# Kernel tuning notes

Hardware: AMD Instinct MI355X
Metric: run time of the kernel (lower is better)

Reference implementation:

```python
import jax, jax.numpy as jnp
import numpy as np

N, DEG, IN_DIM, HID, OUT = 50000, 32, 256, 256, 128

def setup_inputs() -> dict:
    key = jax.random.key(0)
    k1, k2, k3, k4, k5, k6 = jax.random.split(key, 6)
    node_features = jax.random.normal(k1, (N, IN_DIM), dtype=jnp.float32)
    neighbor_idx = jax.random.randint(k2, (N, DEG), 0, N)
    scale1 = 1.0 / np.sqrt(2 * IN_DIM)
    scale2 = 1.0 / np.sqrt(HID)
    W1 = jax.random.normal(k3, (HID, 2 * IN_DIM), dtype=jnp.float32) * scale1
    b1 = jax.random.normal(k4, (HID,), dtype=jnp.float32) * scale1
    W2 = jax.random.normal(k5, (OUT, HID), dtype=jnp.float32) * scale2
    b2 = jax.random.normal(k6, (OUT,), dtype=jnp.float32) * scale2
    return {"node_features": node_features, "neighbor_idx": neighbor_idx,
            "W1": W1, "b1": b1, "W2": W2, "b2": b2}

def reference(node_features, neighbor_idx, W1, b1, W2, b2):
    # Layer 0 (mean aggregator, with neighbors):
    # gather [N, DEG, IN_DIM] neighbor features, mean over DEG
    nbr_mean = jnp.mean(node_features[neighbor_idx], axis=1)  # [N, IN_DIM]
    combined = jnp.concatenate([node_features, nbr_mean], axis=-1)  # [N, 2*IN_DIM]
    h = jax.nn.relu(combined @ W1.T + b1)  # [N, HID]
    # Layer 1: empty neighbor list -> linear_without_neighbors + relu
    out = jax.nn.relu(h @ W2.T + b2)  # [N, OUT]
    return out
```

## Files before the change

### kernel.cpp

```cpp
#include <hip/hip_runtime.h>
#include <stdint.h>

#define N_NODES 50000
#define DEG     32
#define IN_DIM  256
#define K1      512
#define HID     256
#define OUT_DIM 128

#define NCHUNK  4
#define CDIM    64
#define SLICE8  ((size_t)N_NODES * CDIM)
#define GT      16

#define MT2    64
#define NT2B   ((N_NODES + MT2 - 1) / MT2)
#define KC2    32
#define NKA    16
#define NKB    8
#define HSTR2  264

typedef __bf16 bf16x8 __attribute__((ext_vector_type(8)));
typedef float  f32x4  __attribute__((ext_vector_type(4)));
typedef float  f32x2  __attribute__((ext_vector_type(2)));

__device__ __forceinline__ unsigned short f2bf(float f) {
    union { float f; unsigned u; } v; v.f = f;
    unsigned r = v.u + 0x7fffu + ((v.u >> 16) & 1u);
    return (unsigned short)(r >> 16);
}
__device__ __forceinline__ int clampN(int v) {
    return v < 0 ? 0 : (v >= N_NODES ? N_NODES - 1 : v);
}
__device__ __forceinline__ void async_copy16(const void* g, void* l) {
    __builtin_amdgcn_global_load_lds(
        (const __attribute__((address_space(1))) void*)g,
        (__attribute__((address_space(3))) void*)l, 16, 0, 0);
}

#define FEAT_BLKS ((N_NODES + 7) / 8)
__global__ __launch_bounds__(256)
void prep_all(const float* __restrict__ feat,
              const float* __restrict__ W1, const float* __restrict__ W2,
              const int*   __restrict__ nbr,
              unsigned short* __restrict__ featb,
              unsigned char*  __restrict__ featF8,
              unsigned short* __restrict__ W1b, unsigned short* __restrict__ W2b,
              unsigned short* __restrict__ nbr16)
{
    const int t = threadIdx.x;
    if (blockIdx.x < FEAT_BLKS) {
        const int node = blockIdx.x * 8 + (t >> 5);
        const int seg  = t & 31;
        if (node < N_NODES) {
            const float4* src = (const float4*)(feat + (size_t)node * IN_DIM + seg * 8);
            float4 f0 = src[0], f1 = src[1];
            ushort4 o0, o1;
            o0.x = f2bf(f0.x); o0.y = f2bf(f0.y); o0.z = f2bf(f0.z); o0.w = f2bf(f0.w);
            o1.x = f2bf(f1.x); o1.y = f2bf(f1.y); o1.z = f2bf(f1.z); o1.w = f2bf(f1.w);
            unsigned short* db = featb + (size_t)node * IN_DIM + seg * 8;
            *(ushort4*)db       = o0;
            *(ushort4*)(db + 4) = o1;
            int u0 = 0, u1 = 0;
            u0 = __builtin_amdgcn_cvt_pk_fp8_f32(f0.x, f0.y, u0, false);
            u0 = __builtin_amdgcn_cvt_pk_fp8_f32(f0.z, f0.w, u0, true);
            u1 = __builtin_amdgcn_cvt_pk_fp8_f32(f1.x, f1.y, u1, false);
            u1 = __builtin_amdgcn_cvt_pk_fp8_f32(f1.z, f1.w, u1, true);
            const int c   = seg >> 3;
            const int off = (seg & 7) * 8;
            unsigned char* d8 = featF8 + (size_t)c * SLICE8 + (size_t)node * CDIM + off;
            ((int*)d8)[0] = u0;
            ((int*)d8)[1] = u1;
        }
    } else {
        const int bid = blockIdx.x - FEAT_BLKS;
        const int stride = 256 * 256 * 4;
        const int tid4 = (bid * 256 + t) * 4;
        for (int i = tid4; i < HID * K1; i += stride) {
            float4 f = *(const float4*)(W1 + i);
            ushort4 o; o.x = f2bf(f.x); o.y = f2bf(f.y); o.z = f2bf(f.z); o.w = f2bf(f.w);
            *(ushort4*)(W1b + i) = o;
        }
        for (int i = tid4; i < OUT_DIM * HID; i += stride) {
            float4 f = *(const float4*)(W2 + i);
            ushort4 o; o.x = f2bf(f.x); o.y = f2bf(f.y); o.z = f2bf(f.z); o.w = f2bf(f.w);
            *(ushort4*)(W2b + i) = o;
        }
        for (int i = tid4; i < N_NODES * DEG; i += stride) {
            int4 v = *(const int4*)(nbr + i);
            ushort4 o;
            o.x = (unsigned short)clampN(v.x); o.y = (unsigned short)clampN(v.y);
            o.z = (unsigned short)clampN(v.z); o.w = (unsigned short)clampN(v.w);
            *(ushort4*)(nbr16 + i) = o;
        }
    }
}

__global__ __launch_bounds__(256)
void gather_mean_fp8(const unsigned char*  __restrict__ featF8,
                     const unsigned short* __restrict__ nbr16,
                     unsigned short*       __restrict__ meanb)
{
    __shared__ unsigned short sIdx[GT * DEG];
    const int tid  = threadIdx.x;
    const int c    = blockIdx.y;
    const int base = blockIdx.x * GT;

    if (tid < 128) {
        *(ushort4*)(sIdx + tid * 4) =
            *(const ushort4*)(nbr16 + (size_t)base * DEG + tid * 4);
    }
    __syncthreads();

    const unsigned char* slice = featF8 + (size_t)c * SLICE8;
    const int grp = tid >> 4;
    const int ln  = tid & 15;
    const unsigned short* idxr = sIdx + grp * DEG;

    unsigned vv[DEG];
    #pragma unroll
    for (int j = 0; j < DEG; ++j) {
        int nb = idxr[j];
        vv[j] = *(const unsigned*)(slice + (size_t)nb * CDIM + ln * 4);
    }
    float s0 = 0.f, s1 = 0.f, s2 = 0.f, s3 = 0.f;
    #pragma unroll
    for (int j = 0; j < DEG; ++j) {
        f32x2 lo = __builtin_amdgcn_cvt_pk_f32_fp8(vv[j], false);
        f32x2 hi = __builtin_amdgcn_cvt_pk_f32_fp8(vv[j], true);
        s0 += lo[0]; s1 += lo[1]; s2 += hi[0]; s3 += hi[1];
    }
    const float sc = 1.0f / 32.0f;
    ushort4 o;
    o.x = f2bf(s0 * sc); o.y = f2bf(s1 * sc);
    o.z = f2bf(s2 * sc); o.w = f2bf(s3 * sc);
    const int node = base + grp;
    *(ushort4*)(meanb + (size_t)node * IN_DIM + c * CDIM + ln * 4) = o;
}

__global__ __launch_bounds__(512, 2)
void sage_gemm3(const unsigned short* __restrict__ featb,
                const unsigned short* __restrict__ meanb,
                const unsigned short* __restrict__ W1b,
                const float*          __restrict__ b1,
                const unsigned short* __restrict__ W2b,
                const float*          __restrict__ b2,
                float*                __restrict__ out)
{
    __shared__ __align__(16) unsigned short sA[2][MT2 * KC2];
    __shared__ __align__(16) unsigned short sW[2][256 * KC2];
    __shared__ __align__(16) unsigned short sH[MT2 * HSTR2];

    const int tid  = threadIdx.x;
    const int lane = tid & 63;
    const int wave = tid >> 6;
    const int r    = lane & 15;
    const int q    = lane >> 4;
    const int mh   = wave >> 2;
    const int nq   = wave & 3;
    const int nh   = wave & 3;

    const int tbase = blockIdx.x * MT2;

    const int srow = lane >> 2;
    const int sg   = (lane & 3) ^ (srow & 3);

    auto stageA = [&](int kc, int b) {
        if (wave < 4) {
            const int row  = wave * 16 + srow;
            const int node = clampN(tbase + row);
            const unsigned short* basep = (kc < 8) ? featb : meanb;
            async_copy16(basep + (size_t)node * IN_DIM + (kc & 7) * KC2 + sg * 8,
                         &sA[b][wave * 16 * KC2]);
        }
    };
    auto stageW1 = [&](int kc, int b) {
        #pragma unroll
        for (int j = 0; j < 2; ++j) {
            const int n = wave * 32 + j * 16 + srow;
            async_copy16(W1b + (size_t)n * K1 + kc * KC2 + sg * 8,
                         &sW[b][(wave * 32 + j * 16) * KC2]);
        }
    };
    auto stageW2 = [&](int c, int b) {
        const int n = wave * 16 + srow;
        async_copy16(W2b + (size_t)n * HID + c * KC2 + sg * 8,
                     &sW[b][(wave * 16) * KC2]);
    };

    f32x4 acc1[2][4];
    #pragma unroll
    for (int mt = 0; mt < 2; ++mt)
        #pragma unroll
        for (int nt = 0; nt < 4; ++nt)
            acc1[mt][nt] = (f32x4){0.f, 0.f, 0.f, 0.f};

    stageA(0, 0); stageW1(0, 0);
    __syncthreads();
    int buf = 0;
    for (int kc = 0; kc < NKA; ++kc) {
        if (kc + 1 < NKA) { stageA(kc + 1, buf ^ 1); stageW1(kc + 1, buf ^ 1); }
        else              { stageW2(0, buf ^ 1); }
        {
            const int sl = (q ^ (r & 3)) * 8;
            bf16x8 a[2], w[4];
            #pragma unroll
            for (int mt = 0; mt < 2; ++mt)
                a[mt] = *(const bf16x8*)(&sA[buf][(mh * 32 + mt * 16 + r) * KC2 + sl]);
            #pragma unroll
            for (int nt = 0; nt < 4; ++nt)
                w[nt] = *(const bf16x8*)(&sW[buf][(nq * 64 + nt * 16 + r) * KC2 + sl]);
            #pragma unroll
            for (int mt = 0; mt < 2; ++mt)
                #pragma unroll
                for (int nt = 0; nt < 4; ++nt)
                    acc1[mt][nt] = __builtin_amdgcn_mfma_f32_16x16x32_bf16(
                        a[mt], w[nt], acc1[mt][nt], 0, 0, 0);
        }
        __syncthreads();
        buf ^= 1;
    }

    #pragma unroll
    for (int nt = 0; nt < 4; ++nt) {
        const int n = nq * 64 + nt * 16 + r;
        const float bias = b1[n];
        #pragma unroll
        for (int mt = 0; mt < 2; ++mt)
            #pragma unroll
            for (int g = 0; g < 4; ++g) {
                const int m = mh * 32 + mt * 16 + q * 4 + g;
                float v = acc1[mt][nt][g] + bias;
                sH[m * HSTR2 + n] = f2bf(v > 0.f ? v : 0.f);
            }
    }
    __syncthreads();

    f32x4 acc2[2][2];
    #pragma unroll
    for (int mt = 0; mt < 2; ++mt)
        #pragma unroll
        for (int nt = 0; nt < 2; ++nt)
            acc2[mt][nt] = (f32x4){0.f, 0.f, 0.f, 0.f};

    for (int c = 0; c < NKB; ++c) {
        if (c + 1 < NKB) stageW2(c + 1, buf ^ 1);
        {
            const int sl = (q ^ (r & 3)) * 8;
            bf16x8 h[2], w2[2];
            #pragma unroll
            for (int mt = 0; mt < 2; ++mt)
                h[mt] = *(const bf16x8*)(&sH[(mh * 32 + mt * 16 + r) * HSTR2
                                             + c * KC2 + q * 8]);
            #pragma unroll
            for (int nt = 0; nt < 2; ++nt)
                w2[nt] = *(const bf16x8*)(&sW[buf][(nh * 32 + nt * 16 + r) * KC2 + sl]);
            #pragma unroll
            for (int mt = 0; mt < 2; ++mt)
                #pragma unroll
                for (int nt = 0; nt < 2; ++nt)
                    acc2[mt][nt] = __builtin_amdgcn_mfma_f32_16x16x32_bf16(
                        h[mt], w2[nt], acc2[mt][nt], 0, 0, 0);
        }
        __syncthreads();
        buf ^= 1;
    }

    #pragma unroll
    for (int nt = 0; nt < 2; ++nt) {
        const int o = nh * 32 + nt * 16 + r;
        const float bias = b2[o];
        #pragma unroll
        for (int mt = 0; mt < 2; ++mt)
            #pragma unroll
            for (int g = 0; g < 4; ++g) {
                const int m = mh * 32 + mt * 16 + q * 4 + g;
                const int node = tbase + m;
                if (node < N_NODES) {
                    float v = acc2[mt][nt][g] + bias;
                    out[(size_t)node * OUT_DIM + o] = v > 0.f ? v : 0.f;
                }
            }
    }
}

__global__ __launch_bounds__(256)
void sage_naive(const float* __restrict__ feat, const int* __restrict__ nbr,
                const float* __restrict__ W1, const float* __restrict__ b1,
                const float* __restrict__ W2, const float* __restrict__ b2,
                float* __restrict__ out) {
    __shared__ float comb[K1];
    __shared__ float h[HID];
    const int node = blockIdx.x;
    const int t = threadIdx.x;
    comb[t] = feat[(size_t)node * IN_DIM + t];
    float acc = 0.f;
    for (int d = 0; d < DEG; ++d) {
        int nb = clampN(nbr[node * DEG + d]);
        acc += feat[(size_t)nb * IN_DIM + t];
    }
    comb[IN_DIM + t] = acc * (1.0f / 32.0f);
    __syncthreads();
    float s = b1[t];
    for (int k = 0; k < K1; ++k) s += comb[k] * W1[(size_t)t * K1 + k];
    h[t] = s > 0.f ? s : 0.f;
    __syncthreads();
    if (t < OUT_DIM) {
        float s2 = b2[t];
        for (int k = 0; k < HID; ++k) s2 += h[k] * W2[(size_t)t * HID + k];
        out[(size_t)node * OUT_DIM + t] = s2 > 0.f ? s2 : 0.f;
    }
}

extern "C" void kernel_launch(void* const* d_in, const int* in_sizes, int n_in,
                              void* d_out, int out_size, void* d_ws, size_t ws_size,
                              hipStream_t stream) {
    const float* feat = (const float*)d_in[0];
    const int*   nbr  = (const int*)d_in[1];
    const float* W1   = (const float*)d_in[2];
    const float* b1   = (const float*)d_in[3];
    const float* W2   = (const float*)d_in[4];
    const float* b2   = (const float*)d_in[5];
    float* out = (float*)d_out;

    const size_t feat_elems = (size_t)N_NODES * IN_DIM;
    const size_t w1_elems   = (size_t)HID * K1;
    const size_t w2_elems   = (size_t)OUT_DIM * HID;
    const size_t mean_elems = (size_t)N_NODES * IN_DIM;
    const size_t idx_elems  = (size_t)N_NODES * DEG;
    const size_t u16_elems  = feat_elems + w1_elems + w2_elems + mean_elems + idx_elems;
    const size_t need = u16_elems * sizeof(unsigned short)
                      + (size_t)NCHUNK * SLICE8;

    if (ws_size >= need) {
        unsigned short* featb  = (unsigned short*)d_ws;
        unsigned short* W1b    = featb + feat_elems;
        unsigned short* W2b    = W1b + w1_elems;
        unsigned short* meanb  = W2b + w2_elems;
        unsigned short* nbr16  = meanb + mean_elems;
        unsigned char*  featF8 = (unsigned char*)(nbr16 + idx_elems);

        prep_all<<<FEAT_BLKS + 256, 256, 0, stream>>>(feat, W1, W2, nbr,
                                                      featb, featF8, W1b, W2b, nbr16);
        gather_mean_fp8<<<dim3(N_NODES / GT, NCHUNK), 256, 0, stream>>>(featF8, nbr16, meanb);
        sage_gemm3<<<NT2B, 512, 0, stream>>>(featb, meanb, W1b, b1, W2b, b2, out);
    } else {
        sage_naive<<<N_NODES, 256, 0, stream>>>(feat, nbr, W1, b1, W2, b2, out);
    }
}
```

Before: 178.6 us.

## Widen GEMM K-chunk to 64 and hand-schedule async pipeline with explicit waitcnts

The fused two-layer GEMM kernel now stages K in chunks of 64 instead of 32, using an 8-way XOR swizzle so every wave participates in loading A. The main loop is fully unrolled and uses explicit s_waitcnt vmcnt and s_barrier in place of __syncthreads, so the next chunk's global-to-LDS loads can stay in flight during compute. Bias values are preloaded into registers at kernel start. LDS usage doubles and launch bounds drop to one block per CU, which lowers occupancy. The hand-counted vmcnt values also risk races if the compiler emits other vector memory ops.

```diff
diff --git a/kernel.cpp b/kernel.cpp
--- a/kernel.cpp
+++ b/kernel.cpp
@@ -15,14 +15,17 @@
 
 #define MT2    64
 #define NT2B   ((N_NODES + MT2 - 1) / MT2)
-#define KC2    32
-#define NKA    16
-#define NKB    8
+#define KC3    64
 #define HSTR2  264
 
 typedef __bf16 bf16x8 __attribute__((ext_vector_type(8)));
 typedef float  f32x4  __attribute__((ext_vector_type(4)));
 typedef float  f32x2  __attribute__((ext_vector_type(2)));
+
+#define PIN(x)   asm volatile("" : "+v"(x))
+#define WAITV(N) asm volatile("s_waitcnt vmcnt(" #N ")" ::: "memory")
+#define WAITL()  asm volatile("s_waitcnt lgkmcnt(0)" ::: "memory")
+#define BAR()    asm volatile("s_barrier" ::: "memory")
 
 __device__ __forceinline__ unsigned short f2bf(float f) {
     union { float f; unsigned u; } v; v.f = f;
@@ -138,8 +141,8 @@
     *(ushort4*)(meanb + (size_t)node * IN_DIM + c * CDIM + ln * 4) = o;
 }
 
-__global__ __launch_bounds__(512, 2)
-void sage_gemm3(const unsigned short* __restrict__ featb,
+__global__ __launch_bounds__(512, 1)
+void sage_gemm4(const unsigned short* __restrict__ featb,
                 const unsigned short* __restrict__ meanb,
                 const unsigned short* __restrict__ W1b,
                 const float*          __restrict__ b1,
@@ -147,8 +150,8 @@
                 const float*          __restrict__ b2,
                 float*                __restrict__ out)
 {
-    __shared__ __align__(16) unsigned short sA[2][MT2 * KC2];
-    __shared__ __align__(16) unsigned short sW[2][256 * KC2];
+    __shared__ __align__(16) unsigned short sA[2][MT2 * KC3];
+    __shared__ __align__(16) unsigned short sW[2][256 * KC3];
     __shared__ __align__(16) unsigned short sH[MT2 * HSTR2];
 
     const int tid  = threadIdx.x;
@@ -159,33 +162,39 @@
     const int mh   = wave >> 2;
     const int nq   = wave & 3;
     const int nh   = wave & 3;
+    const int lrow = lane >> 3;
+    const int lsl  = lane & 7;
 
     const int tbase = blockIdx.x * MT2;
 
-    const int srow = lane >> 2;
-    const int sg   = (lane & 3) ^ (srow & 3);
+    float bias1[4], bias2v[2];
+    #pragma unroll
+    for (int nt = 0; nt < 4; ++nt) { bias1[nt] = b1[nq * 64 + nt * 16 + r]; PIN(bias1[nt]); }
+    #pragma unroll
+    for (int nt = 0; nt < 2; ++nt) { bias2v[nt] = b2[nh * 32 + nt * 16 + r]; PIN(bias2v[nt]); }
 
     auto stageA = [&](int kc, int b) {
-        if (wave < 4) {
-            const int row  = wave * 16 + srow;
-            const int node = clampN(tbase + row);
-            const unsigned short* basep = (kc < 8) ? featb : meanb;
-            async_copy16(basep + (size_t)node * IN_DIM + (kc & 7) * KC2 + sg * 8,
-                         &sA[b][wave * 16 * KC2]);
-        }
+        const int p    = wave * 8 + lrow;
+        const int node = clampN(tbase + p);
+        const unsigned short* basep = (kc < 4) ? featb : meanb;
+        async_copy16(basep + (size_t)node * IN_DIM + (kc & 3) * KC3 + ((lsl ^ (p & 7)) << 3),
+                     &sA[b][wave * 8 * KC3]);
     };
     auto stageW1 = [&](int kc, int b) {
         #pragma unroll
+        for (int j = 0; j < 4; ++j) {
+            const int n = wave * 32 + j * 8 + lrow;
+            async_copy16(W1b + (size_t)n * K1 + kc * KC3 + ((lsl ^ (n & 7)) << 3),
+                         &sW[b][(wave * 32 + j * 8) * KC3]);
+        }
+    };
+    auto stageW2 = [&](int c, int b) {
+        #pragma unroll
         for (int j = 0; j < 2; ++j) {
-            const int n = wave * 32 + j * 16 + srow;
-            async_copy16(W1b + (size_t)n * K1 + kc * KC2 + sg * 8,
-                         &sW[b][(wave * 32 + j * 16) * KC2]);
-        }
-    };
-    auto stageW2 = [&](int c, int b) {
-        const int n = wave * 16 + srow;
-        async_copy16(W2b + (size_t)n * HID + c * KC2 + sg * 8,
-                     &sW[b][(wave * 16) * KC2]);
+            const int n = wave * 16 + j * 8 + lrow;
+            async_copy16(W2b + (size_t)n * HID + c * KC3 + ((lsl ^ (n & 7)) << 3),
+                         &sW[b][(wave * 16 + j * 8) * KC3]);
+        }
     };
 
     f32x4 acc1[2][4];
@@ -195,21 +204,17 @@
         for (int nt = 0; nt < 4; ++nt)
             acc1[mt][nt] = (f32x4){0.f, 0.f, 0.f, 0.f};
 
-    stageA(0, 0); stageW1(0, 0);
-    __syncthreads();
-    int buf = 0;
-    for (int kc = 0; kc < NKA; ++kc) {
-        if (kc + 1 < NKA) { stageA(kc + 1, buf ^ 1); stageW1(kc + 1, buf ^ 1); }
-        else              { stageW2(0, buf ^ 1); }
-        {
-            const int sl = (q ^ (r & 3)) * 8;
+    auto computeA = [&](int b) {
+        #pragma unroll
+        for (int kk = 0; kk < 2; ++kk) {
+            const int sl = ((kk * 4 + q) ^ (r & 7)) * 8;
             bf16x8 a[2], w[4];
             #pragma unroll
             for (int mt = 0; mt < 2; ++mt)
-                a[mt] = *(const bf16x8*)(&sA[buf][(mh * 32 + mt * 16 + r) * KC2 + sl]);
+                a[mt] = *(const bf16x8*)(&sA[b][(mh * 32 + mt * 16 + r) * KC3 + sl]);
             #pragma unroll
             for (int nt = 0; nt < 4; ++nt)
-                w[nt] = *(const bf16x8*)(&sW[buf][(nq * 64 + nt * 16 + r) * KC2 + sl]);
+                w[nt] = *(const bf16x8*)(&sW[b][(nq * 64 + nt * 16 + r) * KC3 + sl]);
             #pragma unroll
             for (int mt = 0; mt < 2; ++mt)
                 #pragma unroll
@@ -217,24 +222,7 @@
                     acc1[mt][nt] = __builtin_amdgcn_mfma_f32_16x16x32_bf16(
                         a[mt], w[nt], acc1[mt][nt], 0, 0, 0);
         }
-        __syncthreads();
-        buf ^= 1;
-    }
-
-    #pragma unroll
-    for (int nt = 0; nt < 4; ++nt) {
-        const int n = nq * 64 + nt * 16 + r;
-        const float bias = b1[n];
-        #pragma unroll
-        for (int mt = 0; mt < 2; ++mt)
-            #pragma unroll
-            for (int g = 0; g < 4; ++g) {
-                const int m = mh * 32 + mt * 16 + q * 4 + g;
-                float v = acc1[mt][nt][g] + bias;
-                sH[m * HSTR2 + n] = f2bf(v > 0.f ? v : 0.f);
-            }
-    }
-    __syncthreads();
+    };
 
     f32x4 acc2[2][2];
     #pragma unroll
@@ -243,18 +231,18 @@
         for (int nt = 0; nt < 2; ++nt)
             acc2[mt][nt] = (f32x4){0.f, 0.f, 0.f, 0.f};
 
-    for (int c = 0; c < NKB; ++c) {
-        if (c + 1 < NKB) stageW2(c + 1, buf ^ 1);
-        {
-            const int sl = (q ^ (r & 3)) * 8;
+    auto computeB = [&](int c, int b) {
+        #pragma unroll
+        for (int kk = 0; kk < 2; ++kk) {
+            const int sl = ((kk * 4 + q) ^ (r & 7)) * 8;
             bf16x8 h[2], w2[2];
             #pragma unroll
             for (int mt = 0; mt < 2; ++mt)
                 h[mt] = *(const bf16x8*)(&sH[(mh * 32 + mt * 16 + r) * HSTR2
-                                             + c * KC2 + q * 8]);
+                                             + c * KC3 + kk * 32 + q * 8]);
             #pragma unroll
             for (int nt = 0; nt < 2; ++nt)
-                w2[nt] = *(const bf16x8*)(&sW[buf][(nh * 32 + nt * 16 + r) * KC2 + sl]);
+                w2[nt] = *(const bf16x8*)(&sW[b][(nh * 32 + nt * 16 + r) * KC3 + sl]);
             #pragma unroll
             for (int mt = 0; mt < 2; ++mt)
                 #pragma unroll
@@ -262,14 +250,43 @@
                     acc2[mt][nt] = __builtin_amdgcn_mfma_f32_16x16x32_bf16(
                         h[mt], w2[nt], acc2[mt][nt], 0, 0, 0);
         }
-        __syncthreads();
-        buf ^= 1;
-    }
+    };
+
+    stageA(0, 0); stageW1(0, 0);
+    stageA(1, 1); stageW1(1, 1);
+
+    WAITV(5); BAR(); computeA(0); WAITL(); BAR(); stageA(2, 0); stageW1(2, 0);
+    WAITV(5); BAR(); computeA(1); WAITL(); BAR(); stageA(3, 1); stageW1(3, 1);
+    WAITV(5); BAR(); computeA(0); WAITL(); BAR(); stageA(4, 0); stageW1(4, 0);
+    WAITV(5); BAR(); computeA(1); WAITL(); BAR(); stageA(5, 1); stageW1(5, 1);
+    WAITV(5); BAR(); computeA(0); WAITL(); BAR(); stageA(6, 0); stageW1(6, 0);
+    WAITV(5); BAR(); computeA(1); WAITL(); BAR(); stageA(7, 1); stageW1(7, 1);
+    WAITV(5); BAR(); computeA(0); WAITL(); BAR(); stageW2(0, 0);
+    WAITV(2); BAR(); computeA(1); WAITL(); BAR(); stageW2(1, 1);
+
+    #pragma unroll
+    for (int nt = 0; nt < 4; ++nt) {
+        const int n = nq * 64 + nt * 16 + r;
+        #pragma unroll
+        for (int mt = 0; mt < 2; ++mt)
+            #pragma unroll
+            for (int g = 0; g < 4; ++g) {
+                const int m = mh * 32 + mt * 16 + q * 4 + g;
+                float v = acc1[mt][nt][g] + bias1[nt];
+                sH[m * HSTR2 + n] = f2bf(v > 0.f ? v : 0.f);
+            }
+    }
+    WAITL();
+    WAITV(2); BAR();
+
+    computeB(0, 0); WAITL(); BAR(); stageW2(2, 0);
+    WAITV(2); BAR(); computeB(1, 1); WAITL(); BAR(); stageW2(3, 1);
+    WAITV(2); BAR(); computeB(2, 0);
+    WAITV(0); BAR(); computeB(3, 1);
 
     #pragma unroll
     for (int nt = 0; nt < 2; ++nt) {
         const int o = nh * 32 + nt * 16 + r;
-        const float bias = b2[o];
         #pragma unroll
         for (int mt = 0; mt < 2; ++mt)
             #pragma unroll
@@ -277,7 +294,7 @@
                 const int m = mh * 32 + mt * 16 + q * 4 + g;
                 const int node = tbase + m;
                 if (node < N_NODES) {
-                    float v = acc2[mt][nt][g] + bias;
+                    float v = acc2[mt][nt][g] + bias2v[nt];
                     out[(size_t)node * OUT_DIM + o] = v > 0.f ? v : 0.f;
                 }
             }
@@ -343,7 +360,7 @@
         prep_all<<<FEAT_BLKS + 256, 256, 0, stream>>>(feat, W1, W2, nbr,
                                                       featb, featF8, W1b, W2b, nbr16);
         gather_mean_fp8<<<dim3(N_NODES / GT, NCHUNK), 256, 0, stream>>>(featF8, nbr16, meanb);
-        sage_gemm3<<<NT2B, 512, 0, stream>>>(featb, meanb, W1b, b1, W2b, b2, out);
+        sage_gemm4<<<NT2B, 512, 0, stream>>>(featb, meanb, W1b, b1, W2b, b2, out);
     } else {
         sage_naive<<<N_NODES, 256, 0, stream>>>(feat, nbr, W1, b1, W2, b2, out);
     }
```

New measurement: 182.5 us. 2.1% more time.

## Shrink fused GEMM tile to 32 rows, drop double buffering for occupancy

Applied to the files above, without the earlier changes.

The fused two-layer GEMM kernel now uses 32-node tiles with 256 threads (4 waves, each owning a column slice) instead of 64-node tiles with 512 threads, and replaces the double-buffered LDS pipeline with single-buffered load-sync-compute steps. The aim is lower LDS use per block so more blocks fit per CU, with latency hidden by other blocks rather than prefetching. In exchange, the W1 and W2 weight tiles are reloaded from global memory twice as often per node, and each k-step now waits on its own loads.

```diff
diff --git a/kernel.cpp b/kernel.cpp
--- a/kernel.cpp
+++ b/kernel.cpp
@@ -13,11 +13,11 @@
 #define SLICE8  ((size_t)N_NODES * CDIM)
 #define GT      16
 
-#define MT2    64
-#define NT2B   ((N_NODES + MT2 - 1) / MT2)
-#define KC2    32
-#define NKA    16
-#define NKB    8
+#define MT3    32
+#define NT3B   ((N_NODES + MT3 - 1) / MT3)
+#define KC4    32
+#define NKA3   16
+#define NKB3   8
 #define HSTR2  264
 
 typedef __bf16 bf16x8 __attribute__((ext_vector_type(8)));
@@ -138,8 +138,8 @@
     *(ushort4*)(meanb + (size_t)node * IN_DIM + c * CDIM + ln * 4) = o;
 }
 
-__global__ __launch_bounds__(512, 2)
-void sage_gemm3(const unsigned short* __restrict__ featb,
+__global__ __launch_bounds__(256, 4)
+void sage_gemm5(const unsigned short* __restrict__ featb,
                 const unsigned short* __restrict__ meanb,
                 const unsigned short* __restrict__ W1b,
                 const float*          __restrict__ b1,
@@ -147,69 +147,54 @@
                 const float*          __restrict__ b2,
                 float*                __restrict__ out)
 {
-    __shared__ __align__(16) unsigned short sA[2][MT2 * KC2];
-    __shared__ __align__(16) unsigned short sW[2][256 * KC2];
-    __shared__ __align__(16) unsigned short sH[MT2 * HSTR2];
+    __shared__ __align__(16) unsigned short sA[MT3 * KC4];
+    __shared__ __align__(16) unsigned short sW[256 * KC4];
+    __shared__ __align__(16) unsigned short sH[MT3 * HSTR2];
 
     const int tid  = threadIdx.x;
     const int lane = tid & 63;
     const int wave = tid >> 6;
     const int r    = lane & 15;
     const int q    = lane >> 4;
-    const int mh   = wave >> 2;
-    const int nq   = wave & 3;
-    const int nh   = wave & 3;
-
-    const int tbase = blockIdx.x * MT2;
-
     const int srow = lane >> 2;
-    const int sg   = (lane & 3) ^ (srow & 3);
-
-    auto stageA = [&](int kc, int b) {
-        if (wave < 4) {
+    const int sg   = lane & 3;
+
+    const int tbase = blockIdx.x * MT3;
+
+    f32x4 acc1[2][4];
+    #pragma unroll
+    for (int mt = 0; mt < 2; ++mt)
+        #pragma unroll
+        for (int nt = 0; nt < 4; ++nt)
+            acc1[mt][nt] = (f32x4){0.f, 0.f, 0.f, 0.f};
+
+    for (int kc = 0; kc < NKA3; ++kc) {
+        #pragma unroll
+        for (int j = 0; j < 4; ++j) {
+            const int rbase = wave * 64 + j * 16;
+            const int row   = rbase + srow;
+            async_copy16(W1b + (size_t)row * K1 + kc * KC4 + ((sg ^ (row & 3)) << 3),
+                         &sW[rbase * KC4]);
+        }
+        if (wave < 2) {
             const int row  = wave * 16 + srow;
             const int node = clampN(tbase + row);
             const unsigned short* basep = (kc < 8) ? featb : meanb;
-            async_copy16(basep + (size_t)node * IN_DIM + (kc & 7) * KC2 + sg * 8,
-                         &sA[b][wave * 16 * KC2]);
-        }
-    };
-    auto stageW1 = [&](int kc, int b) {
-        #pragma unroll
-        for (int j = 0; j < 2; ++j) {
-            const int n = wave * 32 + j * 16 + srow;
-            async_copy16(W1b + (size_t)n * K1 + kc * KC2 + sg * 8,
-                         &sW[b][(wave * 32 + j * 16) * KC2]);
-        }
-    };
-    auto stageW2 = [&](int c, int b) {
-        const int n = wave * 16 + srow;
-        async_copy16(W2b + (size_t)n * HID + c * KC2 + sg * 8,
-                     &sW[b][(wave * 16) * KC2]);
-    };
-
-    f32x4 acc1[2][4];
-    #pragma unroll
-    for (int mt = 0; mt < 2; ++mt)
-        #pragma unroll
-        for (int nt = 0; nt < 4; ++nt)
-            acc1[mt][nt] = (f32x4){0.f, 0.f, 0.f, 0.f};
-
-    stageA(0, 0); stageW1(0, 0);
-    __syncthreads();
-    int buf = 0;
-    for (int kc = 0; kc < NKA; ++kc) {
-        if (kc + 1 < NKA) { stageA(kc + 1, buf ^ 1); stageW1(kc + 1, buf ^ 1); }
-        else              { stageW2(0, buf ^ 1); }
+            async_copy16(basep + (size_t)node * IN_DIM + (kc & 7) * KC4
+                             + ((sg ^ (row & 3)) << 3),
+                         &sA[wave * 16 * KC4]);
+        }
+        __syncthreads();
+
         {
             const int sl = (q ^ (r & 3)) * 8;
             bf16x8 a[2], w[4];
             #pragma unroll
             for (int mt = 0; mt < 2; ++mt)
-                a[mt] = *(const bf16x8*)(&sA[buf][(mh * 32 + mt * 16 + r) * KC2 + sl]);
+                a[mt] = *(const bf16x8*)(&sA[(mt * 16 + r) * KC4 + sl]);
             #pragma unroll
             for (int nt = 0; nt < 4; ++nt)
-                w[nt] = *(const bf16x8*)(&sW[buf][(nq * 64 + nt * 16 + r) * KC2 + sl]);
+                w[nt] = *(const bf16x8*)(&sW[(wave * 64 + nt * 16 + r) * KC4 + sl]);
             #pragma unroll
             for (int mt = 0; mt < 2; ++mt)
                 #pragma unroll
@@ -218,23 +203,21 @@
                         a[mt], w[nt], acc1[mt][nt], 0, 0, 0);
         }
         __syncthreads();
-        buf ^= 1;
     }
 
     #pragma unroll
     for (int nt = 0; nt < 4; ++nt) {
-        const int n = nq * 64 + nt * 16 + r;
+        const int n = wave * 64 + nt * 16 + r;
         const float bias = b1[n];
         #pragma unroll
         for (int mt = 0; mt < 2; ++mt)
             #pragma unroll
             for (int g = 0; g < 4; ++g) {
-                const int m = mh * 32 + mt * 16 + q * 4 + g;
+                const int m = mt * 16 + q * 4 + g;
                 float v = acc1[mt][nt][g] + bias;
                 sH[m * HSTR2 + n] = f2bf(v > 0.f ? v : 0.f);
             }
     }
-    __syncthreads();
 
     f32x4 acc2[2][2];
     #pragma unroll
@@ -243,18 +226,25 @@
         for (int nt = 0; nt < 2; ++nt)
             acc2[mt][nt] = (f32x4){0.f, 0.f, 0.f, 0.f};
 
-    for (int c = 0; c < NKB; ++c) {
-        if (c + 1 < NKB) stageW2(c + 1, buf ^ 1);
+    for (int c = 0; c < NKB3; ++c) {
+        #pragma unroll
+        for (int j = 0; j < 2; ++j) {
+            const int rbase = wave * 32 + j * 16;
+            const int row   = rbase + srow;
+            async_copy16(W2b + (size_t)row * HID + c * KC4 + ((sg ^ (row & 3)) << 3),
+                         &sW[rbase * KC4]);
+        }
+        __syncthreads();
+
         {
             const int sl = (q ^ (r & 3)) * 8;
             bf16x8 h[2], w2[2];
             #pragma unroll
             for (int mt = 0; mt < 2; ++mt)
-                h[mt] = *(const bf16x8*)(&sH[(mh * 32 + mt * 16 + r) * HSTR2
-                                             + c * KC2 + q * 8]);
+                h[mt] = *(const bf16x8*)(&sH[(mt * 16 + r) * HSTR2 + c * KC4 + q * 8]);
             #pragma unroll
             for (int nt = 0; nt < 2; ++nt)
-                w2[nt] = *(const bf16x8*)(&sW[buf][(nh * 32 + nt * 16 + r) * KC2 + sl]);
+                w2[nt] = *(const bf16x8*)(&sW[(wave * 32 + nt * 16 + r) * KC4 + sl]);
             #pragma unroll
             for (int mt = 0; mt < 2; ++mt)
                 #pragma unroll
@@ -263,18 +253,17 @@
                         h[mt], w2[nt], acc2[mt][nt], 0, 0, 0);
         }
         __syncthreads();
-        buf ^= 1;
     }
 
     #pragma unroll
     for (int nt = 0; nt < 2; ++nt) {
-        const int o = nh * 32 + nt * 16 + r;
+        const int o = wave * 32 + nt * 16 + r;
         const float bias = b2[o];
         #pragma unroll
         for (int mt = 0; mt < 2; ++mt)
             #pragma unroll
             for (int g = 0; g < 4; ++g) {
-                const int m = mh * 32 + mt * 16 + q * 4 + g;
+                const int m = mt * 16 + q * 4 + g;
                 const int node = tbase + m;
                 if (node < N_NODES) {
                     float v = acc2[mt][nt][g] + bias;
@@ -343,7 +332,7 @@
         prep_all<<<FEAT_BLKS + 256, 256, 0, stream>>>(feat, W1, W2, nbr,
                                                       featb, featF8, W1b, W2b, nbr16);
         gather_mean_fp8<<<dim3(N_NODES / GT, NCHUNK), 256, 0, stream>>>(featF8, nbr16, meanb);
-        sage_gemm3<<<NT2B, 512, 0, stream>>>(featb, meanb, W1b, b1, W2b, b2, out);
+        sage_gemm5<<<NT3B, 256, 0, stream>>>(featb, meanb, W1b, b1, W2b, b2, out);
     } else {
         sage_naive<<<N_NODES, 256, 0, stream>>>(feat, nbr, W1, b1, W2, b2, out);
     }
```

Measured after the change: 184.7 us. +3.4%, slower.
